# Kernel tuning notes

Measured on AMD Instinct MI355X. Metric: run time of the kernel, lower is better.

Reference implementation:

```python
import math
import jax, jax.numpy as jnp
import numpy as np

N = 131072   # flattened batch (agents * timesteps)
D = 4        # input_dim
F = 64       # num_freq_bands
H = 128      # hidden_dim
EPS = 1e-5


def _layer_norm(x, g, b):
    mu = jnp.mean(x, axis=-1, keepdims=True)
    var = jnp.var(x, axis=-1, keepdims=True)
    return (x - mu) * jax.lax.rsqrt(var + EPS) * g + b


def setup_inputs() -> dict:
    key = jax.random.key(0)
    ks = jax.random.split(key, 8)
    fin = 2 * F + 1  # 129
    return {
        "continuous_inputs": jax.random.normal(ks[0], (N, D), dtype=jnp.float32),
        "freqs": jax.random.normal(ks[1], (D, F), dtype=jnp.float32),
        # per-dim MLP ensemble, stacked over D
        "w1": jax.random.normal(ks[2], (D, fin, H), dtype=jnp.float32) * (1.0 / math.sqrt(fin)),
        "b1": jnp.zeros((D, H), dtype=jnp.float32),
        "ln1_g": jnp.ones((D, H), dtype=jnp.float32),
        "ln1_b": jnp.zeros((D, H), dtype=jnp.float32),
        "w2": jax.random.normal(ks[3], (D, H, H), dtype=jnp.float32) * (1.0 / math.sqrt(H)),
        "b2": jnp.zeros((D, H), dtype=jnp.float32),
        # to_out head
        "out_ln_g": jnp.ones((H,), dtype=jnp.float32),
        "out_ln_b": jnp.zeros((H,), dtype=jnp.float32),
        "w3": jax.random.normal(ks[4], (H, H), dtype=jnp.float32) * (1.0 / math.sqrt(H)),
        "b3": jnp.zeros((H,), dtype=jnp.float32),
    }


def reference(continuous_inputs, freqs, w1, b1, ln1_g, ln1_b, w2, b2,
              out_ln_g, out_ln_b, w3, b3):
    # x: [N, D, F] = input[..., None] * freqs * 2*pi
    x = continuous_inputs[..., None] * freqs * (2.0 * math.pi)
    # Fourier features: [N, D, 2F+1]
    feat = jnp.concatenate([jnp.cos(x), jnp.sin(x), continuous_inputs[..., None]], axis=-1)
    # batched per-dim MLP: Linear -> LayerNorm -> ReLU -> Linear, then sum over D
    h = jnp.einsum("ndf,dfh->ndh", feat, w1) + b1          # [N, D, H]
    h = _layer_norm(h, ln1_g, ln1_b)
    h = jax.nn.relu(h)
    h = jnp.einsum("ndh,dhk->ndk", h, w2) + b2             # [N, D, H]
    emb = jnp.sum(h, axis=1)                               # [N, H]
    # to_out: LayerNorm -> ReLU -> Linear
    out = _layer_norm(emb, out_ln_g, out_ln_b)
    out = jax.nn.relu(out)
    return out @ w3 + b3
```

## Files before the change

kernel.cpp:

```cpp
#include <hip/hip_runtime.h>
#include <hip/hip_bf16.h>
#include <math.h>

typedef __bf16 bf16t;
typedef __bf16 bf8v __attribute__((ext_vector_type(8)));
typedef float  f4v  __attribute__((ext_vector_type(4)));
typedef unsigned int u32;
typedef u32 u4v __attribute__((ext_vector_type(4)));

#define DD  4
#define FF  64
#define HH  128
#define FIN 129
#define MT  128

#define AS1 __attribute__((address_space(1)))
#define AS3 __attribute__((address_space(3)))

#define P_FREQS 0
#define P_B1    256
#define P_W1L   768
#define P_G1    1280
#define P_BB1   1792
#define P_B2    2304
#define P_OG    2816
#define P_OB    2944
#define P_B3    3072
#define P_TOT   3200

__device__ __forceinline__ int swz(int row, int k) {
  return row * HH + ((((k >> 3) ^ (row & 7)) << 3) | (k & 7));
}

__device__ __forceinline__ int hinv(int k) {
  return (k & ~31) | (((k >> 2) & 3) << 3) | (((k >> 4) & 1) << 2) | (k & 3);
}

__global__ void prep_weights(const float* __restrict__ w1,
                             const float* __restrict__ w2,
                             const float* __restrict__ w3,
                             bf16t* __restrict__ w1t,
                             bf16t* __restrict__ w2t,
                             bf16t* __restrict__ w3t,
                             float* __restrict__ w1last) {
  int i = blockIdx.x * blockDim.x + threadIdx.x;
  if (i < DD * FIN * HH) {
    int n = i & 127, dk = i >> 7, k = dk % FIN, d = dk / FIN;
    float v = w1[i];
    if (k == 128) w1last[d * HH + n] = v;
    else          w1t[(d * HH + n) * HH + k] = (bf16t)v;
  }
  if (i < DD * HH * HH) {
    int n = i & 127, k = (i >> 7) & 127, d = i >> 14;
    w2t[(d * HH + n) * HH + hinv(k)] = (bf16t)w2[i];
  }
  if (i < HH * HH) {
    int n = i & 127, k = i >> 7;
    w3t[n * HH + hinv(k)] = (bf16t)w3[i];
  }
}

__device__ __forceinline__ void stage_w_async(const bf16t* __restrict__ w,
                                              bf16t* __restrict__ ldsW,
                                              int tid, int wave) {
  int g0 = (tid & ~15) | ((tid & 15) ^ ((tid >> 4) & 7));
  const bf16t* src = w + g0 * 8;
  bf16t* dst = ldsW + wave * 64 * 8;
  #pragma unroll
  for (int j = 0; j < 8; ++j) {
    __builtin_amdgcn_global_load_lds((const AS1 void*)(src + j * 2048),
                                     (AS3 void*)(dst + j * 2048), 16, 0, 0);
  }
}

__device__ __forceinline__ u32 pack2(float a, float b) {
  union { bf16t h; unsigned short u; } ua, ub;
  ua.h = (bf16t)a; ub.h = (bf16t)b;
  return ((u32)ub.u << 16) | (u32)ua.u;
}

__device__ __forceinline__ void pack_frag(const f4v (&h)[8], bf8v (&bb)[4]) {
  #pragma unroll
  for (int K = 0; K < 4; ++K) {
    u4v wv;
    wv.x = pack2(h[2 * K][0],     h[2 * K][1]);
    wv.y = pack2(h[2 * K][2],     h[2 * K][3]);
    wv.z = pack2(h[2 * K + 1][0], h[2 * K + 1][1]);
    wv.w = pack2(h[2 * K + 1][2], h[2 * K + 1][3]);
    union { u4v w; bf8v v; } cv;
    cv.w = wv;
    bb[K] = cv.v;
  }
}

#define VM_SYNC(N) do {                                        \
    asm volatile("s_waitcnt vmcnt(" #N ")" ::: "memory");      \
    __builtin_amdgcn_s_barrier();                              \
  } while (0)
#define BAR() __builtin_amdgcn_s_barrier()

__launch_bounds__(256, 2)
__global__ void fourier_mlp(
    const float* __restrict__ cont,
    const float* __restrict__ freqs,
    const float* __restrict__ b1,
    const float* __restrict__ ln1g,
    const float* __restrict__ ln1b,
    const float* __restrict__ b2,
    const float* __restrict__ outg,
    const float* __restrict__ outb,
    const float* __restrict__ b3,
    const bf16t* __restrict__ w1t,
    const bf16t* __restrict__ w2t,
    const bf16t* __restrict__ w3t,
    const float* __restrict__ w1last,
    float* __restrict__ out)
{
  __shared__ __align__(16) bf16t ldsW0[HH * HH];
  __shared__ __align__(16) bf16t ldsW1[HH * HH];
  __shared__ __align__(16) float ldsP[P_TOT];

  const int tid  = threadIdx.x;
  const int lane = tid & 63;
  const int wave = tid >> 6;
  const int q    = lane >> 4;
  const int l15  = lane & 15;
  const int rowbase = blockIdx.x * MT;
  const int wrow = wave * 32;

  f4v call[2];
  call[0] = *(const f4v*)&cont[(rowbase + wrow + l15) * DD];
  call[1] = *(const f4v*)&cont[(rowbase + wrow + 16 + l15) * DD];

  stage_w_async(w1t, ldsW0, tid, wave);
  ldsP[P_FREQS + tid] = freqs[tid];
  #pragma unroll
  for (int i = 0; i < 2; ++i) {
    int j = tid + i * 256;
    ldsP[P_B1 + j]  = b1[j];
    ldsP[P_W1L + j] = w1last[j];
    ldsP[P_G1 + j]  = ln1g[j];
    ldsP[P_BB1 + j] = ln1b[j];
    ldsP[P_B2 + j]  = b2[j];
  }
  if (tid < 128) {
    ldsP[P_OG + tid] = outg[tid];
    ldsP[P_OB + tid] = outb[tid];
    ldsP[P_B3 + tid] = b3[tid];
  }

  const f4v fzero = {0.0f, 0.0f, 0.0f, 0.0f};
  f4v emb[2][8];
  #pragma unroll
  for (int g = 0; g < 2; ++g)
    #pragma unroll
    for (int nt = 0; nt < 8; ++nt) emb[g][nt] = fzero;

  __syncthreads();

  for (int d = 0; d < DD; ++d) {
    stage_w_async(w2t + d * HH * HH, ldsW1, tid, wave);

    bf8v fB[2][4];
    #pragma unroll
    for (int g = 0; g < 2; ++g) {
      const float c = call[g][d];
      #pragma unroll
      for (int hf = 0; hf < 2; ++hf) {
        f4v f0 = *(const f4v*)&ldsP[P_FREQS + d * FF + hf * 32 + q * 8];
        f4v f1 = *(const f4v*)&ldsP[P_FREQS + d * FF + hf * 32 + q * 8 + 4];
        #pragma unroll
        for (int u = 0; u < 8; ++u) {
          float fv = (u < 4) ? f0[u] : f1[u - 4];
          float a = c * fv;
          float t = a - floorf(a);
          fB[g][hf][u]     = (bf16t)__builtin_amdgcn_cosf(t);
          fB[g][2 + hf][u] = (bf16t)__builtin_amdgcn_sinf(t);
        }
      }
    }
    VM_SYNC(8);

    f4v acc[2][8];
    #pragma unroll
    for (int g = 0; g < 2; ++g)
      #pragma unroll
      for (int nt = 0; nt < 8; ++nt) acc[g][nt] = fzero;
    #pragma unroll
    for (int K = 0; K < 4; ++K)
      #pragma unroll
      for (int nt = 0; nt < 8; ++nt) {
        bf8v wf = *(const bf8v*)&ldsW0[swz(nt * 16 + l15, K * 32 + q * 8)];
        acc[0][nt] = __builtin_amdgcn_mfma_f32_16x16x32_bf16(wf, fB[0][K], acc[0][nt], 0, 0, 0);
        acc[1][nt] = __builtin_amdgcn_mfma_f32_16x16x32_bf16(wf, fB[1][K], acc[1][nt], 0, 0, 0);
      }
    BAR();

    stage_w_async(d < 3 ? (w1t + (d + 1) * HH * HH) : w3t, ldsW0, tid, wave);

    bf8v bB[2][4];
    #pragma unroll
    for (int g = 0; g < 2; ++g) {
      const float c = call[g][d];
      float s = 0.0f, ss = 0.0f;
      #pragma unroll
      for (int nt = 0; nt < 8; ++nt) {
        f4v b1v = *(const f4v*)&ldsP[P_B1 + d * HH + nt * 16 + q * 4];
        f4v w1l = *(const f4v*)&ldsP[P_W1L + d * HH + nt * 16 + q * 4];
        #pragma unroll
        for (int r = 0; r < 4; ++r) {
          float v = acc[g][nt][r] + b1v[r] + c * w1l[r];
          acc[g][nt][r] = v;
          s += v; ss += v * v;
        }
      }
      s  += __shfl_xor(s, 16);  s  += __shfl_xor(s, 32);
      ss += __shfl_xor(ss, 16); ss += __shfl_xor(ss, 32);
      float mu   = s * (1.0f / 128.0f);
      float var  = ss * (1.0f / 128.0f) - mu * mu;
      float rstd = rsqrtf(var + 1e-5f);
      #pragma unroll
      for (int nt = 0; nt < 8; ++nt) {
        f4v gv = *(const f4v*)&ldsP[P_G1 + d * HH + nt * 16 + q * 4];
        f4v bv = *(const f4v*)&ldsP[P_BB1 + d * HH + nt * 16 + q * 4];
        #pragma unroll
        for (int r = 0; r < 4; ++r) {
          float v = (acc[g][nt][r] - mu) * rstd * gv[r] + bv[r];
          acc[g][nt][r] = fmaxf(v, 0.0f);
        }
      }
      pack_frag(acc[g], bB[g]);
    }
    VM_SYNC(8);

    #pragma unroll
    for (int K = 0; K < 4; ++K)
      #pragma unroll
      for (int nt = 0; nt < 8; ++nt) {
        bf8v wf = *(const bf8v*)&ldsW1[swz(nt * 16 + l15, K * 32 + q * 8)];
        emb[0][nt] = __builtin_amdgcn_mfma_f32_16x16x32_bf16(wf, bB[0][K], emb[0][nt], 0, 0, 0);
        emb[1][nt] = __builtin_amdgcn_mfma_f32_16x16x32_bf16(wf, bB[1][K], emb[1][nt], 0, 0, 0);
      }
    #pragma unroll
    for (int nt = 0; nt < 8; ++nt) {
      f4v b2v = *(const f4v*)&ldsP[P_B2 + d * HH + nt * 16 + q * 4];
      emb[0][nt] += b2v;
      emb[1][nt] += b2v;
    }
    BAR();
  }

  bf8v bB[2][4];
  #pragma unroll
  for (int g = 0; g < 2; ++g) {
    float s = 0.0f, ss = 0.0f;
    #pragma unroll
    for (int nt = 0; nt < 8; ++nt)
      #pragma unroll
      for (int r = 0; r < 4; ++r) {
        float v = emb[g][nt][r];
        s += v; ss += v * v;
      }
    s  += __shfl_xor(s, 16);  s  += __shfl_xor(s, 32);
    ss += __shfl_xor(ss, 16); ss += __shfl_xor(ss, 32);
    float mu   = s * (1.0f / 128.0f);
    float var  = ss * (1.0f / 128.0f) - mu * mu;
    float rstd = rsqrtf(var + 1e-5f);
    #pragma unroll
    for (int nt = 0; nt < 8; ++nt) {
      f4v gv = *(const f4v*)&ldsP[P_OG + nt * 16 + q * 4];
      f4v bv = *(const f4v*)&ldsP[P_OB + nt * 16 + q * 4];
      #pragma unroll
      for (int r = 0; r < 4; ++r) {
        float v = (emb[g][nt][r] - mu) * rstd * gv[r] + bv[r];
        emb[g][nt][r] = fmaxf(v, 0.0f);
      }
    }
    pack_frag(emb[g], bB[g]);
  }
  VM_SYNC(0);

  f4v acc[2][8];
  #pragma unroll
  for (int g = 0; g < 2; ++g)
    #pragma unroll
    for (int nt = 0; nt < 8; ++nt) acc[g][nt] = fzero;
  #pragma unroll
  for (int K = 0; K < 4; ++K)
    #pragma unroll
    for (int nt = 0; nt < 8; ++nt) {
      bf8v wf = *(const bf8v*)&ldsW0[swz(nt * 16 + l15, K * 32 + q * 8)];
      acc[0][nt] = __builtin_amdgcn_mfma_f32_16x16x32_bf16(wf, bB[0][K], acc[0][nt], 0, 0, 0);
      acc[1][nt] = __builtin_amdgcn_mfma_f32_16x16x32_bf16(wf, bB[1][K], acc[1][nt], 0, 0, 0);
    }

  #pragma unroll
  for (int nt = 0; nt < 8; ++nt) {
    f4v b3v = *(const f4v*)&ldsP[P_B3 + nt * 16 + q * 4];
    #pragma unroll
    for (int g = 0; g < 2; ++g) {
      f4v o = acc[g][nt] + b3v;
      *(f4v*)&out[(rowbase + wrow + g * 16 + l15) * HH + nt * 16 + q * 4] = o;
    }
  }
}

extern "C" void kernel_launch(void* const* d_in, const int* in_sizes, int n_in,
                              void* d_out, int out_size, void* d_ws, size_t ws_size,
                              hipStream_t stream) {
  const float* cont  = (const float*)d_in[0];
  const float* freqs = (const float*)d_in[1];
  const float* w1    = (const float*)d_in[2];
  const float* b1    = (const float*)d_in[3];
  const float* ln1g  = (const float*)d_in[4];
  const float* ln1b  = (const float*)d_in[5];
  const float* w2    = (const float*)d_in[6];
  const float* b2    = (const float*)d_in[7];
  const float* outg  = (const float*)d_in[8];
  const float* outb  = (const float*)d_in[9];
  const float* w3    = (const float*)d_in[10];
  const float* b3    = (const float*)d_in[11];
  float* out = (float*)d_out;

  bf16t* w1t = (bf16t*)d_ws;
  bf16t* w2t = w1t + DD * HH * HH;
  bf16t* w3t = w2t + DD * HH * HH;
  float* w1last = (float*)((char*)d_ws + (2 * DD * HH * HH + HH * HH) * sizeof(bf16t));

  prep_weights<<<(DD * FIN * HH + 255) / 256, 256, 0, stream>>>(
      w1, w2, w3, w1t, w2t, w3t, w1last);

  int n_rows = in_sizes[0] / DD;
  int grid = n_rows / MT;
  fourier_mlp<<<grid, 256, 0, stream>>>(
      cont, freqs, b1, ln1g, ln1b, b2, outg, outb, b3,
      w1t, w2t, w3t, w1last, out);
}
```

Baseline: 168.0 us.

## Switch matrix products from 16x16x32 to 32x32x16 MFMA tiles

Replaces the two 16-row MFMA groups per wave with a single 32x32x16 MFMA tile layout. The fragment mapping, weight permutation, LayerNorm reductions and output stores are all reworked for the new accumulator layout. The aim is to halve the LDS weight fragment loads per MFMA (each weight fragment now serves 32 rows) and to cut the cross-lane shuffles in the reductions. In exchange, the larger MFMA has longer latency and offers fewer independent accumulators to interleave, and the changed lane mappings risk correctness errors.

```diff
diff --git a/kernel.cpp b/kernel.cpp
--- a/kernel.cpp
+++ b/kernel.cpp
@@ -5,6 +5,7 @@
 typedef __bf16 bf16t;
 typedef __bf16 bf8v __attribute__((ext_vector_type(8)));
 typedef float  f4v  __attribute__((ext_vector_type(4)));
+typedef float  f16v __attribute__((ext_vector_type(16)));
 typedef unsigned int u32;
 typedef u32 u4v __attribute__((ext_vector_type(4)));
 
@@ -32,8 +33,8 @@
   return row * HH + ((((k >> 3) ^ (row & 7)) << 3) | (k & 7));
 }
 
-__device__ __forceinline__ int hinv(int k) {
-  return (k & ~31) | (((k >> 2) & 3) << 3) | (((k >> 4) & 1) << 2) | (k & 3);
+__device__ __forceinline__ int hperm32(int k) {
+  return (k & ~12) | ((k & 4) << 1) | ((k & 8) >> 1);
 }
 
 __global__ void prep_weights(const float* __restrict__ w1,
@@ -52,11 +53,11 @@
   }
   if (i < DD * HH * HH) {
     int n = i & 127, k = (i >> 7) & 127, d = i >> 14;
-    w2t[(d * HH + n) * HH + hinv(k)] = (bf16t)w2[i];
+    w2t[(d * HH + n) * HH + hperm32(k)] = (bf16t)w2[i];
   }
   if (i < HH * HH) {
     int n = i & 127, k = i >> 7;
-    w3t[n * HH + hinv(k)] = (bf16t)w3[i];
+    w3t[n * HH + hperm32(k)] = (bf16t)w3[i];
   }
 }
 
@@ -79,18 +80,20 @@
   return ((u32)ub.u << 16) | (u32)ua.u;
 }
 
-__device__ __forceinline__ void pack_frag(const f4v (&h)[8], bf8v (&bb)[4]) {
-  #pragma unroll
-  for (int K = 0; K < 4; ++K) {
-    u4v wv;
-    wv.x = pack2(h[2 * K][0],     h[2 * K][1]);
-    wv.y = pack2(h[2 * K][2],     h[2 * K][3]);
-    wv.z = pack2(h[2 * K + 1][0], h[2 * K + 1][1]);
-    wv.w = pack2(h[2 * K + 1][2], h[2 * K + 1][3]);
-    union { u4v w; bf8v v; } cv;
-    cv.w = wv;
-    bb[K] = cv.v;
-  }
+__device__ __forceinline__ void pack_frag32(const f16v (&h)[4], bf8v (&bb)[8]) {
+  #pragma unroll
+  for (int t = 0; t < 4; ++t)
+    #pragma unroll
+    for (int s = 0; s < 2; ++s) {
+      u4v wv;
+      wv.x = pack2(h[t][8 * s + 0], h[t][8 * s + 1]);
+      wv.y = pack2(h[t][8 * s + 2], h[t][8 * s + 3]);
+      wv.z = pack2(h[t][8 * s + 4], h[t][8 * s + 5]);
+      wv.w = pack2(h[t][8 * s + 6], h[t][8 * s + 7]);
+      union { u4v w; bf8v v; } cv;
+      cv.w = wv;
+      bb[2 * t + s] = cv.v;
+    }
 }
 
 #define VM_SYNC(N) do {                                        \
@@ -123,14 +126,14 @@
   const int tid  = threadIdx.x;
   const int lane = tid & 63;
   const int wave = tid >> 6;
-  const int q    = lane >> 4;
-  const int l15  = lane & 15;
+  const int l31  = lane & 31;
+  const int h    = lane >> 5;
+  const int h8   = h * 8;
+  const int h4   = h * 4;
   const int rowbase = blockIdx.x * MT;
   const int wrow = wave * 32;
 
-  f4v call[2];
-  call[0] = *(const f4v*)&cont[(rowbase + wrow + l15) * DD];
-  call[1] = *(const f4v*)&cont[(rowbase + wrow + 16 + l15) * DD];
+  f4v call = *(const f4v*)&cont[(rowbase + wrow + l31) * DD];
 
   stage_w_async(w1t, ldsW0, tid, wave);
   ldsP[P_FREQS + tid] = freqs[tid];
@@ -149,160 +152,162 @@
     ldsP[P_B3 + tid] = b3[tid];
   }
 
-  const f4v fzero = {0.0f, 0.0f, 0.0f, 0.0f};
-  f4v emb[2][8];
-  #pragma unroll
-  for (int g = 0; g < 2; ++g)
-    #pragma unroll
-    for (int nt = 0; nt < 8; ++nt) emb[g][nt] = fzero;
+  f16v emb[4];
+  #pragma unroll
+  for (int t = 0; t < 4; ++t)
+    #pragma unroll
+    for (int x = 0; x < 16; ++x) emb[t][x] = 0.0f;
 
   __syncthreads();
 
   for (int d = 0; d < DD; ++d) {
     stage_w_async(w2t + d * HH * HH, ldsW1, tid, wave);
 
-    bf8v fB[2][4];
-    #pragma unroll
-    for (int g = 0; g < 2; ++g) {
-      const float c = call[g][d];
-      #pragma unroll
-      for (int hf = 0; hf < 2; ++hf) {
-        f4v f0 = *(const f4v*)&ldsP[P_FREQS + d * FF + hf * 32 + q * 8];
-        f4v f1 = *(const f4v*)&ldsP[P_FREQS + d * FF + hf * 32 + q * 8 + 4];
+    bf8v fB[8];
+    {
+      const float c = call[d];
+      #pragma unroll
+      for (int k2 = 0; k2 < 4; ++k2) {
+        f4v f0 = *(const f4v*)&ldsP[P_FREQS + d * FF + k2 * 16 + h8];
+        f4v f1 = *(const f4v*)&ldsP[P_FREQS + d * FF + k2 * 16 + h8 + 4];
         #pragma unroll
         for (int u = 0; u < 8; ++u) {
           float fv = (u < 4) ? f0[u] : f1[u - 4];
           float a = c * fv;
           float t = a - floorf(a);
-          fB[g][hf][u]     = (bf16t)__builtin_amdgcn_cosf(t);
-          fB[g][2 + hf][u] = (bf16t)__builtin_amdgcn_sinf(t);
+          fB[k2][u]     = (bf16t)__builtin_amdgcn_cosf(t);
+          fB[4 + k2][u] = (bf16t)__builtin_amdgcn_sinf(t);
         }
       }
     }
     VM_SYNC(8);
 
-    f4v acc[2][8];
-    #pragma unroll
-    for (int g = 0; g < 2; ++g)
-      #pragma unroll
-      for (int nt = 0; nt < 8; ++nt) acc[g][nt] = fzero;
-    #pragma unroll
-    for (int K = 0; K < 4; ++K)
-      #pragma unroll
-      for (int nt = 0; nt < 8; ++nt) {
-        bf8v wf = *(const bf8v*)&ldsW0[swz(nt * 16 + l15, K * 32 + q * 8)];
-        acc[0][nt] = __builtin_amdgcn_mfma_f32_16x16x32_bf16(wf, fB[0][K], acc[0][nt], 0, 0, 0);
-        acc[1][nt] = __builtin_amdgcn_mfma_f32_16x16x32_bf16(wf, fB[1][K], acc[1][nt], 0, 0, 0);
+    f16v acc[4];
+    #pragma unroll
+    for (int t = 0; t < 4; ++t)
+      #pragma unroll
+      for (int x = 0; x < 16; ++x) acc[t][x] = 0.0f;
+    #pragma unroll
+    for (int kk = 0; kk < 8; ++kk)
+      #pragma unroll
+      for (int t = 0; t < 4; ++t) {
+        bf8v wf = *(const bf8v*)&ldsW0[swz(t * 32 + l31, kk * 16 + h8)];
+        acc[t] = __builtin_amdgcn_mfma_f32_32x32x16_bf16(wf, fB[kk], acc[t], 0, 0, 0);
       }
     BAR();
 
     stage_w_async(d < 3 ? (w1t + (d + 1) * HH * HH) : w3t, ldsW0, tid, wave);
 
-    bf8v bB[2][4];
-    #pragma unroll
-    for (int g = 0; g < 2; ++g) {
-      const float c = call[g][d];
+    bf8v bB[8];
+    {
+      const float c = call[d];
       float s = 0.0f, ss = 0.0f;
       #pragma unroll
-      for (int nt = 0; nt < 8; ++nt) {
-        f4v b1v = *(const f4v*)&ldsP[P_B1 + d * HH + nt * 16 + q * 4];
-        f4v w1l = *(const f4v*)&ldsP[P_W1L + d * HH + nt * 16 + q * 4];
-        #pragma unroll
-        for (int r = 0; r < 4; ++r) {
-          float v = acc[g][nt][r] + b1v[r] + c * w1l[r];
-          acc[g][nt][r] = v;
-          s += v; ss += v * v;
+      for (int t = 0; t < 4; ++t)
+        #pragma unroll
+        for (int a = 0; a < 4; ++a) {
+          f4v b1v = *(const f4v*)&ldsP[P_B1 + d * HH + t * 32 + a * 8 + h4];
+          f4v w1l = *(const f4v*)&ldsP[P_W1L + d * HH + t * 32 + a * 8 + h4];
+          #pragma unroll
+          for (int r = 0; r < 4; ++r) {
+            float v = acc[t][a * 4 + r] + b1v[r] + c * w1l[r];
+            acc[t][a * 4 + r] = v;
+            s += v; ss += v * v;
+          }
         }
-      }
-      s  += __shfl_xor(s, 16);  s  += __shfl_xor(s, 32);
-      ss += __shfl_xor(ss, 16); ss += __shfl_xor(ss, 32);
+      s  += __shfl_xor(s, 32);
+      ss += __shfl_xor(ss, 32);
       float mu   = s * (1.0f / 128.0f);
       float var  = ss * (1.0f / 128.0f) - mu * mu;
       float rstd = rsqrtf(var + 1e-5f);
       #pragma unroll
-      for (int nt = 0; nt < 8; ++nt) {
-        f4v gv = *(const f4v*)&ldsP[P_G1 + d * HH + nt * 16 + q * 4];
-        f4v bv = *(const f4v*)&ldsP[P_BB1 + d * HH + nt * 16 + q * 4];
-        #pragma unroll
-        for (int r = 0; r < 4; ++r) {
-          float v = (acc[g][nt][r] - mu) * rstd * gv[r] + bv[r];
-          acc[g][nt][r] = fmaxf(v, 0.0f);
+      for (int t = 0; t < 4; ++t)
+        #pragma unroll
+        for (int a = 0; a < 4; ++a) {
+          f4v gv = *(const f4v*)&ldsP[P_G1 + d * HH + t * 32 + a * 8 + h4];
+          f4v bv = *(const f4v*)&ldsP[P_BB1 + d * HH + t * 32 + a * 8 + h4];
+          #pragma unroll
+          for (int r = 0; r < 4; ++r) {
+            float v = (acc[t][a * 4 + r] - mu) * rstd * gv[r] + bv[r];
+            acc[t][a * 4 + r] = fmaxf(v, 0.0f);
+          }
         }
-      }
-      pack_frag(acc[g], bB[g]);
+      pack_frag32(acc, bB);
     }
     VM_SYNC(8);
 
     #pragma unroll
-    for (int K = 0; K < 4; ++K)
-      #pragma unroll
-      for (int nt = 0; nt < 8; ++nt) {
-        bf8v wf = *(const bf8v*)&ldsW1[swz(nt * 16 + l15, K * 32 + q * 8)];
-        emb[0][nt] = __builtin_amdgcn_mfma_f32_16x16x32_bf16(wf, bB[0][K], emb[0][nt], 0, 0, 0);
-        emb[1][nt] = __builtin_amdgcn_mfma_f32_16x16x32_bf16(wf, bB[1][K], emb[1][nt], 0, 0, 0);
-      }
-    #pragma unroll
-    for (int nt = 0; nt < 8; ++nt) {
-      f4v b2v = *(const f4v*)&ldsP[P_B2 + d * HH + nt * 16 + q * 4];
-      emb[0][nt] += b2v;
-      emb[1][nt] += b2v;
-    }
+    for (int kk = 0; kk < 8; ++kk)
+      #pragma unroll
+      for (int t = 0; t < 4; ++t) {
+        bf8v wf = *(const bf8v*)&ldsW1[swz(t * 32 + l31, kk * 16 + h8)];
+        emb[t] = __builtin_amdgcn_mfma_f32_32x32x16_bf16(wf, bB[kk], emb[t], 0, 0, 0);
+      }
+    #pragma unroll
+    for (int t = 0; t < 4; ++t)
+      #pragma unroll
+      for (int a = 0; a < 4; ++a) {
+        f4v b2v = *(const f4v*)&ldsP[P_B2 + d * HH + t * 32 + a * 8 + h4];
+        #pragma unroll
+        for (int r = 0; r < 4; ++r) emb[t][a * 4 + r] += b2v[r];
+      }
     BAR();
   }
 
-  bf8v bB[2][4];
-  #pragma unroll
-  for (int g = 0; g < 2; ++g) {
+  bf8v bB[8];
+  {
     float s = 0.0f, ss = 0.0f;
     #pragma unroll
-    for (int nt = 0; nt < 8; ++nt)
-      #pragma unroll
-      for (int r = 0; r < 4; ++r) {
-        float v = emb[g][nt][r];
+    for (int t = 0; t < 4; ++t)
+      #pragma unroll
+      for (int x = 0; x < 16; ++x) {
+        float v = emb[t][x];
         s += v; ss += v * v;
       }
-    s  += __shfl_xor(s, 16);  s  += __shfl_xor(s, 32);
-    ss += __shfl_xor(ss, 16); ss += __shfl_xor(ss, 32);
+    s  += __shfl_xor(s, 32);
+    ss += __shfl_xor(ss, 32);
     float mu   = s * (1.0f / 128.0f);
     float var  = ss * (1.0f / 128.0f) - mu * mu;
     float rstd = rsqrtf(var + 1e-5f);
     #pragma unroll
-    for (int nt = 0; nt < 8; ++nt) {
-      f4v gv = *(const f4v*)&ldsP[P_OG + nt * 16 + q * 4];
-      f4v bv = *(const f4v*)&ldsP[P_OB + nt * 16 + q * 4];
-      #pragma unroll
-      for (int r = 0; r < 4; ++r) {
-        float v = (emb[g][nt][r] - mu) * rstd * gv[r] + bv[r];
-        emb[g][nt][r] = fmaxf(v, 0.0f);
-      }
-    }
-    pack_frag(emb[g], bB[g]);
+    for (int t = 0; t < 4; ++t)
+      #pragma unroll
+      for (int a = 0; a < 4; ++a) {
+        f4v gv = *(const f4v*)&ldsP[P_OG + t * 32 + a * 8 + h4];
+        f4v bv = *(const f4v*)&ldsP[P_OB + t * 32 + a * 8 + h4];
+        #pragma unroll
+        for (int r = 0; r < 4; ++r) {
+          float v = (emb[t][a * 4 + r] - mu) * rstd * gv[r] + bv[r];
+          emb[t][a * 4 + r] = fmaxf(v, 0.0f);
+        }
+      }
+    pack_frag32(emb, bB);
   }
   VM_SYNC(0);
 
-  f4v acc[2][8];
-  #pragma unroll
-  for (int g = 0; g < 2; ++g)
-    #pragma unroll
-    for (int nt = 0; nt < 8; ++nt) acc[g][nt] = fzero;
-  #pragma unroll
-  for (int K = 0; K < 4; ++K)
-    #pragma unroll
-    for (int nt = 0; nt < 8; ++nt) {
-      bf8v wf = *(const bf8v*)&ldsW0[swz(nt * 16 + l15, K * 32 + q * 8)];
-      acc[0][nt] = __builtin_amdgcn_mfma_f32_16x16x32_bf16(wf, bB[0][K], acc[0][nt], 0, 0, 0);
-      acc[1][nt] = __builtin_amdgcn_mfma_f32_16x16x32_bf16(wf, bB[1][K], acc[1][nt], 0, 0, 0);
-    }
-
-  #pragma unroll
-  for (int nt = 0; nt < 8; ++nt) {
-    f4v b3v = *(const f4v*)&ldsP[P_B3 + nt * 16 + q * 4];
-    #pragma unroll
-    for (int g = 0; g < 2; ++g) {
-      f4v o = acc[g][nt] + b3v;
-      *(f4v*)&out[(rowbase + wrow + g * 16 + l15) * HH + nt * 16 + q * 4] = o;
-    }
-  }
+  f16v acc[4];
+  #pragma unroll
+  for (int t = 0; t < 4; ++t)
+    #pragma unroll
+    for (int x = 0; x < 16; ++x) acc[t][x] = 0.0f;
+  #pragma unroll
+  for (int kk = 0; kk < 8; ++kk)
+    #pragma unroll
+    for (int t = 0; t < 4; ++t) {
+      bf8v wf = *(const bf8v*)&ldsW0[swz(t * 32 + l31, kk * 16 + h8)];
+      acc[t] = __builtin_amdgcn_mfma_f32_32x32x16_bf16(wf, bB[kk], acc[t], 0, 0, 0);
+    }
+
+  #pragma unroll
+  for (int t = 0; t < 4; ++t)
+    #pragma unroll
+    for (int a = 0; a < 4; ++a) {
+      f4v b3v = *(const f4v*)&ldsP[P_B3 + t * 32 + a * 8 + h4];
+      f4v o;
+      #pragma unroll
+      for (int r = 0; r < 4; ++r) o[r] = acc[t][a * 4 + r] + b3v[r];
+      *(f4v*)&out[(rowbase + wrow + l31) * HH + t * 32 + a * 8 + h4] = o;
+    }
 }
 
 extern "C" void kernel_launch(void* const* d_in, const int* in_sizes, int n_in,
```

Result: faster. 160.8 us (-4.3%).
